# Optimization experiments

Measured on AMD Instinct MI355X. Metric: run time of the kernel, lower is better.

The kernel has to match this reference:

```python
import jax, jax.numpy as jnp
import numpy as np

T, N, E, F_IN, H1, H2, NUM_GRAPHS, K = 8, 10000, 320000, 32, 32, 16, 64, 5


def setup_inputs() -> dict:
    key = jax.random.key(0)
    ks = jax.random.split(key, 16)
    p = lambda k, shape: jax.random.normal(k, shape, jnp.float32) * 0.05
    return {
        "x": jax.random.normal(ks[0], (T, N, F_IN), jnp.float32),
        "edge_index": jax.random.randint(ks[1], (2, E), 0, N),
        "edge_attr": jax.random.uniform(ks[2], (E,), jnp.float32),
        "batch": jnp.sort(jax.random.randint(ks[3], (N,), 0, NUM_GRAPHS)),
        "Wx1": p(ks[4], (4, K, F_IN, H1)),
        "bx1": jnp.zeros((4, H1), jnp.float32),
        "Wh1": p(ks[5], (4, K, H1, H1)),
        "bh1": jnp.zeros((4, H1), jnp.float32),
        "wc1": p(ks[6], (3, H1)),
        "b1": jnp.zeros((4, H1), jnp.float32),
        "Wx2": p(ks[7], (4, K, H1, H2)),
        "bx2": jnp.zeros((4, H2), jnp.float32),
        "Wh2": p(ks[8], (4, K, H2, H2)),
        "bh2": jnp.zeros((4, H2), jnp.float32),
        "wc2": p(ks[9], (3, H2)),
        "b2": jnp.zeros((4, H2), jnp.float32),
        "lin_w": p(ks[10], (H2, 1)),
        "lin_b": jnp.zeros((1,), jnp.float32),
    }


def _forward(x, edge_index, edge_attr, batch,
             Wx1, bx1, Wh1, bh1, wc1, b1,
             Wx2, bx2, Wh2, bh2, wc2, b2, lin_w, lin_b):
    src, dst = edge_index[0], edge_index[1]
    n = x.shape[1]

    # ChebConv sym normalization with lambda_max=2: L_hat = L_sym - I = -D^{-1/2} A D^{-1/2}
    deg = jax.ops.segment_sum(edge_attr, src, num_segments=n)
    deg_safe = jnp.where(deg > 0, deg, 1.0)
    dis = jnp.where(deg > 0, jax.lax.rsqrt(deg_safe), 0.0)
    wnorm = dis[src] * edge_attr * dis[dst]  # [E]

    def Lhat(z):  # z: [N, C] -> L_hat @ z
        return -jax.ops.segment_sum(wnorm[:, None] * z[src], dst, num_segments=n)

    def cheb(z, W, b):  # W: [K, C_in, C_out], b: [C_out]
        out = z @ W[0]
        Tp, Tc = z, Lhat(z)  # T_0, T_1
        out = out + Tc @ W[1]
        for k in range(2, W.shape[0]):
            Tp, Tc = Tc, 2.0 * Lhat(Tc) - Tp
            out = out + Tc @ W[k]
        return out + b

    def cell(X, H, C, Wx, bx, Wh, bh, wc, bg):
        # gate order: 0=i, 1=f, 2=c, 3=o (GConvLSTM with peepholes)
        I = jax.nn.sigmoid(cheb(X, Wx[0], bx[0]) + cheb(H, Wh[0], bh[0]) + wc[0] * C + bg[0])
        Fg = jax.nn.sigmoid(cheb(X, Wx[1], bx[1]) + cheb(H, Wh[1], bh[1]) + wc[1] * C + bg[1])
        Ct = jnp.tanh(cheb(X, Wx[2], bx[2]) + cheb(H, Wh[2], bh[2]) + bg[2])
        Cn = Fg * C + I * Ct
        O = jax.nn.sigmoid(cheb(X, Wx[3], bx[3]) + cheb(H, Wh[3], bh[3]) + wc[2] * Cn + bg[3])
        return O * jnp.tanh(Cn), Cn

    @jax.checkpoint
    def step(carry, xt):
        h1, c1, h2, c2 = carry
        h1, c1 = cell(xt, h1, c1, Wx1, bx1, Wh1, bh1, wc1, b1)
        h2, c2 = cell(h1, h2, c2, Wx2, bx2, Wh2, bh2, wc2, b2)
        return (h1, c1, h2, c2), None

    z32 = jnp.zeros((n, Wh1.shape[-1]), x.dtype)
    z16 = jnp.zeros((n, Wh2.shape[-1]), x.dtype)
    (h1, c1, h2, c2), _ = jax.lax.scan(step, (z32, z32, z16, z16), x)

    # relu/dropout on h2 in the torch code is dead code (its result is unused in eval)
    u = jax.ops.segment_sum(h2, batch, num_segments=NUM_GRAPHS)  # global_add_pool
    return (u @ lin_w + lin_b).reshape(-1)


def reference(x, edge_index, edge_attr, batch,
              Wx1, bx1, Wh1, bh1, wc1, b1,
              Wx2, bx2, Wh2, bh2, wc2, b2, lin_w, lin_b):
    return _forward(x, edge_index, edge_attr, batch,
                    Wx1, bx1, Wh1, bh1, wc1, b1,
                    Wx2, bx2, Wh2, bh2, wc2, b2, lin_w, lin_b)
```

## Files before the change

### kernel.cpp

```cpp
#include <hip/hip_runtime.h>
#include <hip/hip_bf16.h>

#define TT 8
#define NN 10000
#define EE 320000
#define NG 64
#define SZH 384

typedef short v8s __attribute__((ext_vector_type(8)));
typedef _Float16 v8h __attribute__((ext_vector_type(8)));
typedef float v4f __attribute__((ext_vector_type(4)));

__device__ __forceinline__ float sigmf(float x){ return 1.f/(1.f+expf(-x)); }
__device__ __forceinline__ unsigned short f2h(float f){ _Float16 h=(_Float16)f; return __builtin_bit_cast(unsigned short,h); }
__device__ __forceinline__ float h2f(unsigned short s){ return (float)__builtin_bit_cast(_Float16,s); }
__device__ __forceinline__ unsigned pack2h(float x,float y){ return (unsigned)f2h(x) | ((unsigned)f2h(y)<<16); }
__device__ __forceinline__ size_t fragidx(int TK,int row,int c){
  int tile=row>>4, m=row&15, kt=c>>5, cc=c&31;
  return ((size_t)(tile*TK+kt)*64 + (cc>>3)*16 + m)*8 + (cc&7);
}

__device__ __forceinline__ float fetchW1(const float* Wx, const float* Wh, int kk, int col){
  int g=col>>5, j=col&31;
  if(kk<160){ int k=kk>>5, i=kk&31; return Wx[((g*5+k)*32+i)*32+j]; }
  int rr=kk-160; int k=rr>>5, i=rr&31; return Wh[((g*5+k)*32+i)*32+j];
}
__device__ __forceinline__ float fetchW2(const float* Wx, const float* Wh, int kk, int col){
  int g=col>>4, j=col&15;
  if(kk<160){ int k=kk>>5, i=kk&31; return Wx[((g*5+k)*32+i)*16+j]; }
  if(kk<240){ int rr=kk-160; int k=rr>>4, i=rr&15; return Wh[((g*5+k)*16+i)*16+j]; }
  return 0.f;
}

__global__ void k_setup0(const int* __restrict__ src, const float* __restrict__ ea, float* __restrict__ deg,
                         const float* __restrict__ Wx1,const float* __restrict__ bx1,
                         const float* __restrict__ Wh1,const float* __restrict__ bh1,const float* __restrict__ b1,
                         const float* __restrict__ Wx2,const float* __restrict__ bx2,
                         const float* __restrict__ Wh2,const float* __restrict__ bh2,const float* __restrict__ b2g,
                         short* __restrict__ Wpk1, short* __restrict__ Wpk2,
                         float* __restrict__ Bc1,float* __restrict__ Bc2,
                         const float* __restrict__ x, unsigned short* __restrict__ ZH, short* __restrict__ Zb1){
  int idx = blockIdx.x*256+threadIdx.x;
  if(idx<EE) atomicAdd(&deg[src[idx]], ea[idx]);
  if(idx < 5120){
    int lane=idx&63, rest=idx>>6;
    int nt=rest&7, kt=rest>>3;
    int col = nt*16 + (lane&15);
    int g = lane>>4;
    #pragma unroll
    for(int j=0;j<8;j++){
      int kk = kt*32 + 8*g + j;
      Wpk1[(size_t)idx*8+j]=(short)f2h(fetchW1(Wx1,Wh1,kk,col));
    }
  } else if(idx < 7168){
    int t=idx-5120;
    int lane=t&63, rest=t>>6;
    int nt=rest&3, kt=rest>>2;
    int col = nt*16 + (lane&15);
    int g = lane>>4;
    #pragma unroll
    for(int j=0;j<8;j++){
      int kk = kt*32 + 8*g + j;
      Wpk2[(size_t)t*8+j]=(short)f2h(fetchW2(Wx2,Wh2,kk,col));
    }
  } else if(idx < 7296){
    int i=idx-7168; int g=i>>5,j=i&31;
    Bc1[i]=bx1[g*32+j]+bh1[g*32+j]+b1[g*32+j];
  } else if(idx < 7360){
    int i=idx-7296; int g=i>>4,j=i&15;
    Bc2[i]=bx2[g*16+j]+bh2[g*16+j]+b2g[g*16+j];
  }
  if(idx<NN*8){
    int n=idx>>3, c4=idx&7;
    float4 v = ((const float4*)x)[idx];
    unsigned p0=pack2h(v.x,v.y), p1=pack2h(v.z,v.w);
    *(unsigned*)&ZH[(size_t)n*SZH + 48 + c4*4]     = p0;
    *(unsigned*)&ZH[(size_t)n*SZH + 48 + c4*4 + 2] = p1;
    size_t fi = fragidx(5, n, c4*4);
    *(unsigned*)&Zb1[fi]   = p0;
    *(unsigned*)&Zb1[fi+2] = p1;
  }
}

__global__ void k_dis(const float* __restrict__ deg, float* __restrict__ dis){
  int n = blockIdx.x*256+threadIdx.x;
  if(n<NN){ float d=deg[n]; dis[n] = d>0.f ? rsqrtf(d) : 0.f; }
}

__global__ void k_wnorm(const int* __restrict__ src, const int* __restrict__ dst, const float* __restrict__ ea,
                        const float* __restrict__ dis, float* __restrict__ wnorm, int* __restrict__ cnt){
  int e = blockIdx.x*256+threadIdx.x;
  if(e<EE){
    int s=src[e], d=dst[e];
    wnorm[e] = dis[s]*ea[e]*dis[d];
    atomicAdd(&cnt[d],1);
  }
}

__global__ __launch_bounds__(1024) void k_scan(const int* __restrict__ cnt, int* __restrict__ rowptr, int* __restrict__ wp){
  __shared__ int wsum[16];
  __shared__ int carrysh;
  int tid=threadIdx.x, lane=tid&63, wv=tid>>6;
  if(tid==0){ carrysh=0; rowptr[0]=0; }
  __syncthreads();
  for(int base=0;base<NN;base+=1024){
    int i=base+tid;
    int v=(i<NN)?cnt[i]:0;
    int s=v;
    #pragma unroll
    for(int d=1;d<64;d<<=1){ int t=__shfl_up(s,d,64); if(lane>=d) s+=t; }
    if(lane==63) wsum[wv]=s;
    __syncthreads();
    if(wv==0 && lane<16){
      int t=wsum[lane]; int ss=t;
      #pragma unroll
      for(int d=1;d<16;d<<=1){ int u=__shfl_up(ss,d,64); if(lane>=d) ss+=u; }
      wsum[lane]=ss-t;
    }
    __syncthreads();
    int total = carrysh + wsum[wv] + s;
    if(i<NN) rowptr[i+1]=total;
    __syncthreads();
    if(tid==1023) carrysh = total;
    __syncthreads();
  }
  for(int i=tid;i<NN;i+=1024) wp[i]=rowptr[i];
}

__global__ void k_scatter(const int* __restrict__ src, const int* __restrict__ dst, const float* __restrict__ wnorm,
                          int* __restrict__ wp, int2* __restrict__ pack){
  int e = blockIdx.x*256+threadIdx.x;
  if(e<EE){
    int d=dst[e];
    int pos = atomicAdd(&wp[d],1);
    pack[pos] = make_int2(src[e], __float_as_int(wnorm[e]));
  }
}

template<int MODE>
__global__ __launch_bounds__(512) void k_spmm(const int* __restrict__ rowptr, const int2* __restrict__ pack,
    unsigned short* __restrict__ ZH,
    short* __restrict__ Zb1, short* __restrict__ Zb2, int k){
  int wlocal = __builtin_amdgcn_readfirstlane(threadIdx.x>>6);
  int wid = blockIdx.x*8 + wlocal;
  if(wid>=NN) return;
  int l = threadIdx.x&63;
  int ch; bool act;
  if(MODE==0){ ch=48+2*l; act=(l<16); }
  else if(MODE==1){
    if(l<16) ch=2*l; else if(l<24) ch=32+2*(l-16); else ch=48+2*(l-24);
    act=(l<40);
  } else {
    if(l<16) ch=2*l; else ch=32+2*(l-16);
    act=(l<24);
  }
  if(!act) ch=(MODE==2)?0:48;
  int cin_h = (k-1)*96 + ch;
  int base,width,cloc;
  if(ch<32){ base=0; width=32; cloc=ch; }
  else if(ch<48){ base=160; width=16; cloc=ch-32; }
  else { base=240; width=32; cloc=ch-48; }
  int cout = base + k*width + cloc;
  const unsigned short* __restrict__ Zc = ZH + cin_h;
  int e0=rowptr[wid], e1=rowptr[wid+1];
  float accx=0.f, accy=0.f;
  int e=e0;
  for(; e+16<=e1; e+=16){
    float w[16]; unsigned z[16];
    #pragma unroll
    for(int j=0;j<16;j++){
      int2 p=pack[e+j];
      w[j]=__int_as_float(p.y);
      z[j]=*(const unsigned*)&Zc[(unsigned)p.x*SZH];
    }
    #pragma unroll
    for(int j=0;j<16;j++){
      accx += h2f((unsigned short)(z[j]&0xffffu))*w[j];
      accy += h2f((unsigned short)(z[j]>>16))*w[j];
    }
  }
  for(; e+4<=e1; e+=4){
    float w[4]; unsigned z[4];
    #pragma unroll
    for(int j=0;j<4;j++){ int2 p=pack[e+j]; w[j]=__int_as_float(p.y); z[j]=*(const unsigned*)&Zc[(unsigned)p.x*SZH]; }
    #pragma unroll
    for(int j=0;j<4;j++){
      accx += h2f((unsigned short)(z[j]&0xffffu))*w[j];
      accy += h2f((unsigned short)(z[j]>>16))*w[j];
    }
  }
  for(; e<e1; ++e){
    int2 p=pack[e];
    unsigned zz=*(const unsigned*)&Zc[(unsigned)p.x*SZH];
    float ww=__int_as_float(p.y);
    accx += h2f((unsigned short)(zz&0xffffu))*ww;
    accy += h2f((unsigned short)(zz>>16))*ww;
  }
  if(act){
    float alpha=(k==1)?1.f:2.f;
    float vx = -alpha*accx, vy = -alpha*accy;
    if(k>=2){
      unsigned pp=*(const unsigned*)&ZH[(size_t)wid*SZH+(k-2)*96+ch];
      vx -= h2f((unsigned short)(pp&0xffffu));
      vy -= h2f((unsigned short)(pp>>16));
    }
    unsigned hh = pack2h(vx,vy);
    if(k<=3) *(unsigned*)&ZH[(size_t)wid*SZH + k*96 + ch] = hh;
    if(ch<48) *(unsigned*)&Zb2[fragidx(8,wid,cout)] = hh;
    else      *(unsigned*)&Zb1[fragidx(5,wid,cout-240)] = hh;
  }
}

__device__ __forceinline__ void gemm1_dev(int tile,int lane,
        const short* __restrict__ Zb1, const short* __restrict__ Zb2,
        const v8s* __restrict__ H1T0r, v8s* __restrict__ H1T0w,
        const short* __restrict__ Wpk, const float* __restrict__ Bc, const float* __restrict__ wc1,
        float* __restrict__ c1, unsigned short* __restrict__ ZH,
        short* __restrict__ Zb1w, const float* __restrict__ xn){
  const v8s* A1=(const v8s*)Zb1 + (size_t)tile*320 + lane;
  const v8s* A2=(const v8s*)Zb2 + (size_t)tile*512 + lane;
  v8h afr[10];
  #pragma unroll
  for(int kt=0;kt<5;kt++) afr[kt]=__builtin_bit_cast(v8h, A1[kt*64]);
  afr[5]=__builtin_bit_cast(v8h, H1T0r[(size_t)tile*64+lane]);
  #pragma unroll
  for(int kt=1;kt<5;kt++) afr[5+kt]=__builtin_bit_cast(v8h, A2[kt*64]);
  const v8s* Wp=(const v8s*)Wpk;
  v4f acc[8];
  #pragma unroll
  for(int nt=0;nt<8;nt++) acc[nt]=(v4f){0.f,0.f,0.f,0.f};
  #pragma unroll
  for(int kt=0;kt<10;kt++){
    #pragma unroll
    for(int nt=0;nt<8;nt++){
      v8h b=__builtin_bit_cast(v8h, Wp[(kt*8+nt)*64+lane]);
      acc[nt]=__builtin_amdgcn_mfma_f32_16x16x32_f16(afr[kt],b,acc[nt],0,0,0);
    }
  }
  int row0=tile*16;
  int j0=lane&15;
  int r0=row0+(lane>>4)*4;
  #pragma unroll
  for(int reg=0;reg<4;reg++){
    int row=r0+reg;
    #pragma unroll
    for(int jj=0;jj<2;jj++){
      int j=jj*16+j0;
      float c=c1[row*32+j];
      float I =sigmf(acc[0+jj][reg]+Bc[j]      + wc1[j]*c);
      float Fg=sigmf(acc[2+jj][reg]+Bc[32+j]   + wc1[32+j]*c);
      float Ct=tanhf(acc[4+jj][reg]+Bc[64+j]);
      float Cn=Fg*c + I*Ct;
      float O =sigmf(acc[6+jj][reg]+Bc[96+j]   + wc1[64+j]*Cn);
      float h =O*tanhf(Cn);
      c1[row*32+j]=Cn;
      ZH[(size_t)row*SZH + j]=f2h(h);
      ((unsigned short*)H1T0w)[fragidx(1,row,j)]=f2h(h);
    }
    if(xn){
      float2 xv=*(const float2*)&xn[(size_t)row*32 + 2*j0];
      unsigned pr=pack2h(xv.x,xv.y);
      *(unsigned*)&ZH[(size_t)row*SZH + 48 + 2*j0]=pr;
      *(unsigned*)&Zb1w[fragidx(5,row,2*j0)]=pr;
    }
  }
}

__device__ __forceinline__ void gemm2_dev(int tile,int lane,
        const short* __restrict__ Zb2, const v8s* __restrict__ H1T0r,
        const short* __restrict__ Wpk, const float* __restrict__ Bc, const float* __restrict__ wc2,
        float* __restrict__ c2, unsigned short* __restrict__ ZH,
        short* __restrict__ Zb2w, float* __restrict__ u, const int* __restrict__ batch, int last){
  const v8s* Az=(const v8s*)Zb2 + (size_t)tile*512 + lane;
  v8h afr[8];
  afr[0]=__builtin_bit_cast(v8h, H1T0r[(size_t)tile*64+lane]);
  #pragma unroll
  for(int kt=1;kt<8;kt++) afr[kt]=__builtin_bit_cast(v8h, Az[kt*64]);
  const v8s* Wp=(const v8s*)Wpk;
  v4f acc[4];
  #pragma unroll
  for(int nt=0;nt<4;nt++) acc[nt]=(v4f){0.f,0.f,0.f,0.f};
  #pragma unroll
  for(int kt=0;kt<8;kt++){
    #pragma unroll
    for(int nt=0;nt<4;nt++){
      v8h b=__builtin_bit_cast(v8h, Wp[(kt*4+nt)*64+lane]);
      acc[nt]=__builtin_amdgcn_mfma_f32_16x16x32_f16(afr[kt],b,acc[nt],0,0,0);
    }
  }
  int row0=tile*16;
  int j=lane&15;
  int r0=row0+(lane>>4)*4;
  #pragma unroll
  for(int reg=0;reg<4;reg++){
    int row=r0+reg;
    float c=c2[row*16+j];
    float I =sigmf(acc[0][reg]+Bc[j]    +wc2[j]*c);
    float Fg=sigmf(acc[1][reg]+Bc[16+j] +wc2[16+j]*c);
    float Ct=tanhf(acc[2][reg]+Bc[32+j]);
    float Cn=Fg*c+I*Ct;
    float O =sigmf(acc[3][reg]+Bc[48+j] +wc2[32+j]*Cn);
    float h =O*tanhf(Cn);
    c2[row*16+j]=Cn;
    ZH[(size_t)row*SZH + 32 + j]=f2h(h);
    Zb2w[fragidx(8,row,160+j)]=(short)f2h(h);
    if(last) atomicAdd(&u[batch[row]*16+j], h);
  }
}

__global__ __launch_bounds__(256) void k_g1(const short* Zb1, const short* Zb2,
        const v8s* H1T0r, v8s* H1T0w, const short* Wpk1, const float* Bc1, const float* wc1,
        float* c1, unsigned short* ZH, short* Zb1w, const float* xn){
  int wv=threadIdx.x>>6, lane=threadIdx.x&63;
  int tile=blockIdx.x*4+wv;
  if(tile>=625) return;
  gemm1_dev(tile,lane,Zb1,Zb2,H1T0r,H1T0w,Wpk1,Bc1,wc1,c1,ZH,Zb1w,xn);
}

__global__ __launch_bounds__(256) void k_g2(const short* Zb2, const v8s* H1T0r,
        const short* Wpk2, const float* Bc2, const float* wc2,
        float* c2, unsigned short* ZH, short* Zb2w,
        float* u, const int* batch, int last){
  int wv=threadIdx.x>>6, lane=threadIdx.x&63;
  int tile=blockIdx.x*4+wv;
  if(tile>=625) return;
  gemm2_dev(tile,lane,Zb2,H1T0r,Wpk2,Bc2,wc2,c2,ZH,Zb2w,u,batch,last);
}

__global__ __launch_bounds__(256) void k_g12(const short* Zb1, const short* Zb2,
        const v8s* H1T0r, v8s* H1T0w,
        const short* Wpk1, const float* Bc1, const float* wc1, float* c1,
        const short* Wpk2, const float* Bc2, const float* wc2, float* c2,
        unsigned short* ZH, short* Zb1w, short* Zb2w,
        const float* xn, float* u, const int* batch){
  int wv=threadIdx.x>>6, lane=threadIdx.x&63;
  if(blockIdx.x<157){
    int tile=blockIdx.x*4+wv;
    if(tile>=625) return;
    gemm1_dev(tile,lane,Zb1,Zb2,H1T0r,H1T0w,Wpk1,Bc1,wc1,c1,ZH,Zb1w,xn);
  } else {
    int tile=(blockIdx.x-157)*4+wv;
    if(tile>=625) return;
    gemm2_dev(tile,lane,Zb2,H1T0r,Wpk2,Bc2,wc2,c2,ZH,Zb2w,u,batch,0);
  }
}

__global__ void k_final(const float* __restrict__ u, const float* __restrict__ lw, const float* __restrict__ lb,
                        float* __restrict__ out){
  int g=threadIdx.x;
  if(g<NG){
    float s=lb[0];
    #pragma unroll
    for(int j=0;j<16;j++) s += u[g*16+j]*lw[j];
    out[g]=s;
  }
}

extern "C" void kernel_launch(void* const* d_in, const int* in_sizes, int n_in,
                              void* d_out, int out_size, void* d_ws, size_t ws_size,
                              hipStream_t stream){
  const float* x   = (const float*)d_in[0];
  const int*   ei  = (const int*)d_in[1];
  const float* ea  = (const float*)d_in[2];
  const int*   bat = (const int*)d_in[3];
  const float* Wx1=(const float*)d_in[4];  const float* bx1=(const float*)d_in[5];
  const float* Wh1=(const float*)d_in[6];  const float* bh1=(const float*)d_in[7];
  const float* wc1=(const float*)d_in[8];  const float* b1 =(const float*)d_in[9];
  const float* Wx2=(const float*)d_in[10]; const float* bx2=(const float*)d_in[11];
  const float* Wh2=(const float*)d_in[12]; const float* bh2=(const float*)d_in[13];
  const float* wc2=(const float*)d_in[14]; const float* b2 =(const float*)d_in[15];
  const float* lw =(const float*)d_in[16]; const float* lb =(const float*)d_in[17];
  const int* src = ei; const int* dst = ei+EE;

  float* ws = (float*)d_ws;
  size_t off=0;
  auto alloc=[&](size_t n)->float*{ float* p=ws+off; off+=(n+15)&~(size_t)15; return p; };
  float* deg=alloc(NN);
  float* c1=alloc((size_t)NN*32);
  float* c2=alloc((size_t)NN*16);
  float* u =alloc(NG*16);
  int*   cnt=(int*)alloc(NN);
  unsigned short* ZH=(unsigned short*)alloc((size_t)NN*SZH/2);
  short* Zb1=(short*)alloc(625*5*64*8/2);
  short* Zb2=(short*)alloc(625*8*64*8/2);
  short* H1T0a=(short*)alloc(625*64*8/2);
  short* H1T0b=(short*)alloc(625*64*8/2);
  size_t zeroEnd=off;
  float* dis=alloc(NN);
  float* wnorm=alloc(EE);
  int*   rowptr=(int*)alloc(NN+1);
  int*   wp=(int*)alloc(NN);
  int2*  pack=(int2*)alloc((size_t)EE*2);
  short* Wpk1=(short*)alloc(5120*4);
  short* Wpk2=(short*)alloc(2048*4);
  float* Bc1=alloc(128);     float* Bc2=alloc(64);
  (void)ws_size; (void)in_sizes; (void)n_in; (void)out_size;
  v8s* H1T0[2] = { (v8s*)H1T0a, (v8s*)H1T0b };

  hipMemsetAsync(d_ws, 0, zeroEnd*sizeof(float), stream);
  k_setup0 <<<1250,256,0,stream>>>(src,ea,deg,
      Wx1,bx1,Wh1,bh1,b1,Wx2,bx2,Wh2,bh2,b2,Wpk1,Wpk2,Bc1,Bc2, x,ZH,Zb1);
  k_dis    <<<40,256,0,stream>>>(deg,dis);
  k_wnorm  <<<1250,256,0,stream>>>(src,dst,ea,dis,wnorm,cnt);
  k_scan   <<<1,1024,0,stream>>>(cnt,rowptr,wp);
  k_scatter<<<1250,256,0,stream>>>(src,dst,wnorm,wp,pack);

  for(int k=1;k<5;k++)
    k_spmm<0><<<1250,512,0,stream>>>(rowptr,pack,ZH,Zb1,Zb2,k);

  k_g1<<<157,256,0,stream>>>(Zb1,Zb2,H1T0[1],H1T0[0],Wpk1,Bc1,wc1,c1,ZH,Zb1, x+(size_t)NN*32);

  for(int t=0;t<TT-1;t++){
    for(int k=1;k<5;k++)
      k_spmm<1><<<1250,512,0,stream>>>(rowptr,pack,ZH,Zb1,Zb2,k);
    k_g12<<<314,256,0,stream>>>(Zb1,Zb2,H1T0[t&1],H1T0[(t+1)&1],
        Wpk1,Bc1,wc1,c1, Wpk2,Bc2,wc2,c2, ZH,Zb1,Zb2,
        (t+2<TT)? x+(size_t)(t+2)*NN*32 : nullptr, u,bat);
  }
  for(int k=1;k<5;k++)
    k_spmm<2><<<1250,512,0,stream>>>(rowptr,pack,ZH,Zb1,Zb2,k);
  k_g2<<<157,256,0,stream>>>(Zb2,H1T0[(TT-1)&1],Wpk2,Bc2,wc2,c2,ZH,Zb2,u,bat,1);

  k_final<<<1,64,0,stream>>>(u,lw,lb,(float*)d_out);
}
```

Measured before the change: 583.4 us.

## Fuse graph preprocessing kernels and use multi-block lookback scan

The in-degree count moves into the setup kernel, and the separate dis and wnorm kernels are folded into the scatter kernel, which now computes the rsqrt normalisation inline. The single-block scan becomes a 10-block decoupled-lookback scan that uses a spin-wait on a zeroed flag array. Packed source indices are pre-multiplied by the row stride so the SpMM gather skips a multiply, and the accumulation uses explicit fmaf. This cuts kernel launches and preprocessing passes, but the lookback spin relies on earlier blocks being scheduled first.

```diff
diff --git a/kernel.cpp b/kernel.cpp
--- a/kernel.cpp
+++ b/kernel.cpp
@@ -32,7 +32,8 @@
   return 0.f;
 }
 
-__global__ void k_setup0(const int* __restrict__ src, const float* __restrict__ ea, float* __restrict__ deg,
+__global__ void k_setup0(const int* __restrict__ src, const int* __restrict__ dst,
+                         const float* __restrict__ ea, float* __restrict__ deg, int* __restrict__ cnt,
                          const float* __restrict__ Wx1,const float* __restrict__ bx1,
                          const float* __restrict__ Wh1,const float* __restrict__ bh1,const float* __restrict__ b1,
                          const float* __restrict__ Wx2,const float* __restrict__ bx2,
@@ -41,7 +42,10 @@
                          float* __restrict__ Bc1,float* __restrict__ Bc2,
                          const float* __restrict__ x, unsigned short* __restrict__ ZH, short* __restrict__ Zb1){
   int idx = blockIdx.x*256+threadIdx.x;
-  if(idx<EE) atomicAdd(&deg[src[idx]], ea[idx]);
+  if(idx<EE){
+    atomicAdd(&deg[src[idx]], ea[idx]);
+    atomicAdd(&cnt[dst[idx]], 1);
+  }
   if(idx < 5120){
     int lane=idx&63, rest=idx>>6;
     int nt=rest&7, kt=rest>>3;
@@ -82,58 +86,58 @@
   }
 }
 
-__global__ void k_dis(const float* __restrict__ deg, float* __restrict__ dis){
-  int n = blockIdx.x*256+threadIdx.x;
-  if(n<NN){ float d=deg[n]; dis[n] = d>0.f ? rsqrtf(d) : 0.f; }
-}
-
-__global__ void k_wnorm(const int* __restrict__ src, const int* __restrict__ dst, const float* __restrict__ ea,
-                        const float* __restrict__ dis, float* __restrict__ wnorm, int* __restrict__ cnt){
+__global__ __launch_bounds__(1024) void k_scan2(const int* __restrict__ cnt, int* __restrict__ rowptr,
+                                                int* __restrict__ wp, int* __restrict__ lookback){
+  __shared__ int wsum[16];
+  __shared__ int blocksum_sh;
+  __shared__ int prevsum_sh;
+  int b=blockIdx.x, tid=threadIdx.x, lane=tid&63, wv=tid>>6;
+  int i = b*1024 + tid;
+  int v = (i<NN)? cnt[i] : 0;
+  int s=v;
+  #pragma unroll
+  for(int d=1;d<64;d<<=1){ int t=__shfl_up(s,d,64); if(lane>=d) s+=t; }
+  if(lane==63) wsum[wv]=s;
+  __syncthreads();
+  if(wv==0 && lane<16){
+    int t=wsum[lane]; int ss=t;
+    #pragma unroll
+    for(int d=1;d<16;d<<=1){ int u=__shfl_up(ss,d,64); if(lane>=d) ss+=u; }
+    wsum[lane]=ss-t;
+  }
+  __syncthreads();
+  int incl = wsum[wv] + s;
+  if(tid==1023) blocksum_sh = incl;
+  __syncthreads();
+  if(tid==0){
+    int prev=0;
+    if(b>0){
+      while(true){ int f=atomicAdd(&lookback[b-1],0); if(f!=0){ prev=f-1; break; } }
+    }
+    atomicExch(&lookback[b], prev + blocksum_sh + 1);
+    prevsum_sh = prev;
+    if(b==0) rowptr[0]=0;
+  }
+  __syncthreads();
+  int prev = prevsum_sh;
+  if(i<NN){
+    rowptr[i+1] = prev + incl;
+    wp[i]       = prev + incl - v;
+  }
+}
+
+__global__ void k_wscatter(const int* __restrict__ src, const int* __restrict__ dst,
+                           const float* __restrict__ ea, const float* __restrict__ deg,
+                           int* __restrict__ wp, int2* __restrict__ pack){
   int e = blockIdx.x*256+threadIdx.x;
   if(e<EE){
     int s=src[e], d=dst[e];
-    wnorm[e] = dis[s]*ea[e]*dis[d];
-    atomicAdd(&cnt[d],1);
-  }
-}
-
-__global__ __launch_bounds__(1024) void k_scan(const int* __restrict__ cnt, int* __restrict__ rowptr, int* __restrict__ wp){
-  __shared__ int wsum[16];
-  __shared__ int carrysh;
-  int tid=threadIdx.x, lane=tid&63, wv=tid>>6;
-  if(tid==0){ carrysh=0; rowptr[0]=0; }
-  __syncthreads();
-  for(int base=0;base<NN;base+=1024){
-    int i=base+tid;
-    int v=(i<NN)?cnt[i]:0;
-    int s=v;
-    #pragma unroll
-    for(int d=1;d<64;d<<=1){ int t=__shfl_up(s,d,64); if(lane>=d) s+=t; }
-    if(lane==63) wsum[wv]=s;
-    __syncthreads();
-    if(wv==0 && lane<16){
-      int t=wsum[lane]; int ss=t;
-      #pragma unroll
-      for(int d=1;d<16;d<<=1){ int u=__shfl_up(ss,d,64); if(lane>=d) ss+=u; }
-      wsum[lane]=ss-t;
-    }
-    __syncthreads();
-    int total = carrysh + wsum[wv] + s;
-    if(i<NN) rowptr[i+1]=total;
-    __syncthreads();
-    if(tid==1023) carrysh = total;
-    __syncthreads();
-  }
-  for(int i=tid;i<NN;i+=1024) wp[i]=rowptr[i];
-}
-
-__global__ void k_scatter(const int* __restrict__ src, const int* __restrict__ dst, const float* __restrict__ wnorm,
-                          int* __restrict__ wp, int2* __restrict__ pack){
-  int e = blockIdx.x*256+threadIdx.x;
-  if(e<EE){
-    int d=dst[e];
+    float ds_=deg[s], dd=deg[d];
+    float is = ds_>0.f ? rsqrtf(ds_) : 0.f;
+    float id = dd >0.f ? rsqrtf(dd ) : 0.f;
+    float w = is*ea[e]*id;
     int pos = atomicAdd(&wp[d],1);
-    pack[pos] = make_int2(src[e], __float_as_int(wnorm[e]));
+    pack[pos] = make_int2(s*SZH, __float_as_int(w));
   }
 }
 
@@ -171,30 +175,30 @@
     for(int j=0;j<16;j++){
       int2 p=pack[e+j];
       w[j]=__int_as_float(p.y);
-      z[j]=*(const unsigned*)&Zc[(unsigned)p.x*SZH];
+      z[j]=*(const unsigned*)&Zc[(unsigned)p.x];
     }
     #pragma unroll
     for(int j=0;j<16;j++){
-      accx += h2f((unsigned short)(z[j]&0xffffu))*w[j];
-      accy += h2f((unsigned short)(z[j]>>16))*w[j];
+      accx = fmaf(h2f((unsigned short)(z[j]&0xffffu)), w[j], accx);
+      accy = fmaf(h2f((unsigned short)(z[j]>>16)),     w[j], accy);
     }
   }
   for(; e+4<=e1; e+=4){
     float w[4]; unsigned z[4];
     #pragma unroll
-    for(int j=0;j<4;j++){ int2 p=pack[e+j]; w[j]=__int_as_float(p.y); z[j]=*(const unsigned*)&Zc[(unsigned)p.x*SZH]; }
+    for(int j=0;j<4;j++){ int2 p=pack[e+j]; w[j]=__int_as_float(p.y); z[j]=*(const unsigned*)&Zc[(unsigned)p.x]; }
     #pragma unroll
     for(int j=0;j<4;j++){
-      accx += h2f((unsigned short)(z[j]&0xffffu))*w[j];
-      accy += h2f((unsigned short)(z[j]>>16))*w[j];
+      accx = fmaf(h2f((unsigned short)(z[j]&0xffffu)), w[j], accx);
+      accy = fmaf(h2f((unsigned short)(z[j]>>16)),     w[j], accy);
     }
   }
   for(; e<e1; ++e){
     int2 p=pack[e];
-    unsigned zz=*(const unsigned*)&Zc[(unsigned)p.x*SZH];
+    unsigned zz=*(const unsigned*)&Zc[(unsigned)p.x];
     float ww=__int_as_float(p.y);
-    accx += h2f((unsigned short)(zz&0xffffu))*ww;
-    accy += h2f((unsigned short)(zz>>16))*ww;
+    accx = fmaf(h2f((unsigned short)(zz&0xffffu)), ww, accx);
+    accy = fmaf(h2f((unsigned short)(zz>>16)),     ww, accy);
   }
   if(act){
     float alpha=(k==1)?1.f:2.f;
@@ -380,14 +384,14 @@
   float* c2=alloc((size_t)NN*16);
   float* u =alloc(NG*16);
   int*   cnt=(int*)alloc(NN);
+  int*   lookback=(int*)alloc(16);
   unsigned short* ZH=(unsigned short*)alloc((size_t)NN*SZH/2);
   short* Zb1=(short*)alloc(625*5*64*8/2);
   short* Zb2=(short*)alloc(625*8*64*8/2);
   short* H1T0a=(short*)alloc(625*64*8/2);
   short* H1T0b=(short*)alloc(625*64*8/2);
   size_t zeroEnd=off;
-  float* dis=alloc(NN);
-  float* wnorm=alloc(EE);
+  float* wnormUNUSED=alloc(16); (void)wnormUNUSED;
   int*   rowptr=(int*)alloc(NN+1);
   int*   wp=(int*)alloc(NN);
   int2*  pack=(int2*)alloc((size_t)EE*2);
@@ -398,12 +402,10 @@
   v8s* H1T0[2] = { (v8s*)H1T0a, (v8s*)H1T0b };
 
   hipMemsetAsync(d_ws, 0, zeroEnd*sizeof(float), stream);
-  k_setup0 <<<1250,256,0,stream>>>(src,ea,deg,
+  k_setup0  <<<1250,256,0,stream>>>(src,dst,ea,deg,cnt,
       Wx1,bx1,Wh1,bh1,b1,Wx2,bx2,Wh2,bh2,b2,Wpk1,Wpk2,Bc1,Bc2, x,ZH,Zb1);
-  k_dis    <<<40,256,0,stream>>>(deg,dis);
-  k_wnorm  <<<1250,256,0,stream>>>(src,dst,ea,dis,wnorm,cnt);
-  k_scan   <<<1,1024,0,stream>>>(cnt,rowptr,wp);
-  k_scatter<<<1250,256,0,stream>>>(src,dst,wnorm,wp,pack);
+  k_scan2   <<<10,1024,0,stream>>>(cnt,rowptr,wp,lookback);
+  k_wscatter<<<1250,256,0,stream>>>(src,dst,ea,deg,wp,pack);
 
   for(int k=1;k<5;k++)
     k_spmm<0><<<1250,512,0,stream>>>(rowptr,pack,ZH,Zb1,Zb2,k);
```

Measured after the change: 573.4 us. About the same (-1.7%).
